# Optimization experiments

Hardware: AMD Instinct MI355X
Metric: run time of the kernel (lower is better)

The kernel has to match this reference:

```python
import jax, jax.numpy as jnp
import numpy as np
from jax import lax

B, N = 4, 5  # batches, cavs per batch (record_len fixed to 5)
SHAPES = [(64, 128, 256), (128, 64, 128), (256, 32, 64)]  # (C,H,W) per scale


def _base_grid(H, W, align_corners):
    if align_corners:
        xs = jnp.linspace(-1.0, 1.0, W)
        ys = jnp.linspace(-1.0, 1.0, H)
    else:
        xs = (jnp.arange(W, dtype=jnp.float32) + 0.5) * (2.0 / W) - 1.0
        ys = (jnp.arange(H, dtype=jnp.float32) + 0.5) * (2.0 / H) - 1.0
    gx, gy = jnp.meshgrid(xs, ys)  # [H,W] each, x varies along W
    return jnp.stack([gx, gy], axis=-1)  # [H,W,2]


def affine_grid(theta, H, W, align_corners):
    # theta: [M,2,3]  -> grid [M,H,W,2], matches torch.F.affine_grid
    base = _base_grid(H, W, align_corners)
    coords = jnp.concatenate([base, jnp.ones((H, W, 1), base.dtype)], axis=-1)  # [H,W,3]
    return jnp.einsum('nij,hwj->nhwi', theta, coords)


def grid_sample(img, grid, align_corners):
    # img [M,C,H,W], grid [M,Hg,Wg,2]; bilinear, zero padding (torch defaults)
    M, C, H, W = img.shape
    gx, gy = grid[..., 0], grid[..., 1]
    if align_corners:
        ix = (gx + 1.0) * 0.5 * (W - 1)
        iy = (gy + 1.0) * 0.5 * (H - 1)
    else:
        ix = ((gx + 1.0) * W - 1.0) * 0.5
        iy = ((gy + 1.0) * H - 1.0) * 0.5
    x0 = jnp.floor(ix); y0 = jnp.floor(iy)
    x1 = x0 + 1.0;      y1 = y0 + 1.0
    wx1 = ix - x0; wx0 = 1.0 - wx1
    wy1 = iy - y0; wy0 = 1.0 - wy1

    def sample_corner(im, xx, yy):
        valid = ((xx >= 0) & (xx < W) & (yy >= 0) & (yy < H)).astype(im.dtype)
        xc = jnp.clip(xx, 0, W - 1).astype(jnp.int32)
        yc = jnp.clip(yy, 0, H - 1).astype(jnp.int32)
        return im[:, yc, xc] * valid[None]  # [C,Hg,Wg]

    def per_image(im, x0_, x1_, y0_, y1_, w00, w01, w10, w11):
        return (sample_corner(im, x0_, y0_) * w00[None]
                + sample_corner(im, x1_, y0_) * w01[None]
                + sample_corner(im, x0_, y1_) * w10[None]
                + sample_corner(im, x1_, y1_) * w11[None])

    return jax.vmap(per_image)(img, x0, x1, y0, y1, wx0 * wy0, wx1 * wy0, wx0 * wy1, wx1 * wy1)


def conv2d(x, w, b, pad):
    y = lax.conv_general_dilated(x, w, (1, 1), [(pad, pad), (pad, pad)],
                                 dimension_numbers=('NCHW', 'OIHW', 'NCHW'))
    return y + b[None, :, None, None]


def instance_norm(x, eps=1e-5):  # torch InstanceNorm2d(affine=False)
    m = jnp.mean(x, axis=(2, 3), keepdims=True)
    v = jnp.var(x, axis=(2, 3), keepdims=True)
    return (x - m) * lax.rsqrt(v + eps)


def leaky(x):
    return jnp.where(x >= 0, x, 0.01 * x)


def setup_inputs():
    key = jax.random.key(0)
    ks = jax.random.split(key, 8)
    out = {}
    for i, (C, H, W) in enumerate(SHAPES):
        out[f'feat{i}'] = jax.random.normal(ks[i], (B * N, C, H, W), dtype=jnp.float32)
    eye = jnp.array([[1., 0., 0.], [0., 1., 0.]], dtype=jnp.float32)
    out['pairwise_t_matrix'] = (jnp.broadcast_to(eye, (B, N, N, 2, 3))
                                + 0.02 * jax.random.normal(ks[3], (B, N, N, 2, 3), dtype=jnp.float32))
    out['record_len'] = jnp.full((B,), N, dtype=jnp.int32)
    C0 = SHAPES[0][0]
    def w(k, shape, fan):
        return jax.random.normal(k, shape, jnp.float32) * (1.0 / np.sqrt(fan))
    out['w1'] = w(ks[4], (32, 2 * C0, 3, 3), 2 * C0 * 9); out['b1'] = jnp.zeros((32,), jnp.float32)
    out['w2'] = w(ks[5], (16, 32, 3, 3), 32 * 9);          out['b2'] = jnp.zeros((16,), jnp.float32)
    out['w3'] = w(ks[6], (8, 16, 1, 1), 16);               out['b3'] = jnp.zeros((8,), jnp.float32)
    out['w4'] = w(ks[7], (2, 8, 1, 1), 8) * 0.1;           out['b4'] = jnp.zeros((2,), jnp.float32)
    return out


def _forward(feat0, feat1, feat2, pairwise_t_matrix, w1, b1, w2, b2, w3, b3, w4, b4):
    feats = [feat0, feat1, feat2]
    # warp every agent into ego (i=0) frame at every scale; warp_affine_simple uses align_corners=True
    theta = pairwise_t_matrix[:, 0, :, :, :].reshape(B * N, 2, 3)
    warped = []
    for f in feats:
        C, H, W = f.shape[1:]
        g = affine_grid(theta, H, W, True)
        warped.append(grid_sample(f, g, True).reshape(B, N, C, H, W))
    C0, H0, W0 = feats[0].shape[1:]
    w0 = warped[0]
    ego = jnp.broadcast_to(w0[:, :1], (B, N - 1, C0, H0, W0))
    cat = jnp.concatenate([ego, w0[:, 1:]], axis=2).reshape(B * (N - 1), 2 * C0, H0, W0)
    # ArbitraryOffset grid net
    x = leaky(instance_norm(conv2d(cat, w1, b1, 1)))
    x = leaky(instance_norm(conv2d(x, w2, b2, 1)))
    x = leaky(instance_norm(conv2d(x, w3, b3, 0)))
    x = conv2d(x, w4, b4, 0)  # [M,2,H0,W0]
    grid_res = x.reshape(B * (N - 1), H0, W0, 2)  # faithful: raw reshape as in the torch source
    grid = grid_res + _base_grid(H0, W0, False)   # identity affine_grid (align_corners=False)
    fused = []
    for s, f in enumerate(warped):
        C, Hs, Ws = f.shape[2:]
        gs = grid[:, ::2 ** s, ::2 ** s, :]  # [M,Hs,Ws,2]
        neigh = f[:, 1:].reshape(B * (N - 1), C, Hs, Ws)
        deformed = grid_sample(neigh, gs, False).reshape(B, N - 1, C, Hs, Ws)
        fused.append(jnp.max(jnp.concatenate([deformed, f[:, :1]], axis=1), axis=1))
    return tuple(fused)


def reference(feat0, feat1, feat2, pairwise_t_matrix, record_len, w1, b1, w2, b2, w3, b3, w4, b4):
    # record_len is fixed to N per batch (constant); kept for signature fidelity
    return _forward(feat0, feat1, feat2, pairwise_t_matrix, w1, b1, w2, b2, w3, b3, w4, b4)
```

## Files before the change

### kernel.cpp

```cpp
#include <hip/hip_runtime.h>


struct Bilin { int i00, i01, i10, i11; float w00, w01, w10, w11; };

__device__ __forceinline__ Bilin make_bilin(float ix, float iy, int W, int H) {
    float x0f = floorf(ix), y0f = floorf(iy);
    float wx1 = ix - x0f, wy1 = iy - y0f;
    float wx0 = 1.f - wx1, wy0 = 1.f - wy1;
    int x0 = (int)x0f, y0 = (int)y0f;
    int x1 = x0 + 1, y1 = y0 + 1;
    bool vx0 = (x0 >= 0 && x0 < W), vx1 = (x1 >= 0 && x1 < W);
    bool vy0 = (y0 >= 0 && y0 < H), vy1 = (y1 >= 0 && y1 < H);
    int cx0 = min(max(x0, 0), W - 1), cx1 = min(max(x1, 0), W - 1);
    int cy0 = min(max(y0, 0), H - 1), cy1 = min(max(y1, 0), H - 1);
    Bilin b;
    b.i00 = cy0 * W + cx0; b.i01 = cy0 * W + cx1;
    b.i10 = cy1 * W + cx0; b.i11 = cy1 * W + cx1;
    b.w00 = (vx0 && vy0) ? wx0 * wy0 : 0.f;
    b.w01 = (vx1 && vy0) ? wx1 * wy0 : 0.f;
    b.w10 = (vx0 && vy1) ? wx0 * wy1 : 0.f;
    b.w11 = (vx1 && vy1) ? wx1 * wy1 : 0.f;
    return b;
}

__global__ __launch_bounds__(256) void warp_kernel(
    const float* __restrict__ src, const float* __restrict__ tmat,
    float* __restrict__ dst, int C, int H, int W)
{
    int idx = blockIdx.x * 256 + threadIdx.x;
    int CGn = C >> 4;
    int HW = H * W;
    int total = 20 * CGn * HW;
    if (idx >= total) return;
    int w   = idx % W;
    int h   = (idx / W) % H;
    int cg  = (idx / HW) % CGn;
    int img = idx / (HW * CGn);
    int b = img / 5, n = img % 5;
    const float* th = tmat + (b * 25 + n) * 6;
    float gx = -1.f + 2.f * w / (float)(W - 1);
    float gy = -1.f + 2.f * h / (float)(H - 1);
    float tx = th[0] * gx + th[1] * gy + th[2];
    float ty = th[3] * gx + th[4] * gy + th[5];
    float ix = (tx + 1.f) * 0.5f * (W - 1);
    float iy = (ty + 1.f) * 0.5f * (H - 1);
    Bilin bl = make_bilin(ix, iy, W, H);
    const float* im = src + ((size_t)img * C + cg * 16) * HW;
    float* op = dst + ((size_t)img * C + cg * 16) * HW + h * W + w;
    #pragma unroll 4
    for (int c = 0; c < 16; ++c) {
        const float* pl = im + c * HW;
        op[c * HW] = pl[bl.i00] * bl.w00 + pl[bl.i01] * bl.w01 +
                     pl[bl.i10] * bl.w10 + pl[bl.i11] * bl.w11;
    }
}

__global__ __launch_bounds__(256) void stats_kernel(
    const float* __restrict__ x, float* __restrict__ stats, int HW)
{
    int pc = blockIdx.x;
    const float* p = x + (size_t)pc * HW;
    float s = 0.f, s2 = 0.f;
    for (int i = threadIdx.x; i < HW; i += 256) {
        float v = p[i];
        s += v; s2 += v * v;
    }
    __shared__ float ss[256], sq[256];
    ss[threadIdx.x] = s; sq[threadIdx.x] = s2;
    __syncthreads();
    for (int o = 128; o > 0; o >>= 1) {
        if (threadIdx.x < o) {
            ss[threadIdx.x] += ss[threadIdx.x + o];
            sq[threadIdx.x] += sq[threadIdx.x + o];
        }
        __syncthreads();
    }
    if (threadIdx.x == 0) {
        float m = ss[0] / HW;
        float var = sq[0] / HW - m * m;
        stats[pc * 2]     = m;
        stats[pc * 2 + 1] = rsqrtf(var + 1e-5f);
    }
}

template<int CIN, int COUT, int WSTRIDE, int SRC, bool INIT, bool NORM>
__global__ __launch_bounds__(256) void conv3x3v2(
    const float* __restrict__ src, const float* __restrict__ wgt,
    const float* __restrict__ bias, const float* __restrict__ stats,
    const float* __restrict__ init, float* __restrict__ dst)
{
    constexpr int H = 128, W = 256, HW = H * W;
    constexpr int CHUNK = 8;
    constexpr int OCP = COUT / 4;
    constexpr int PW = 68;
    __shared__ __align__(16) float s_in[CHUNK][10][PW];
    __shared__ __align__(16) float s_w[CHUNK * 9 * COUT];

    int tid = threadIdx.x;
    int bi  = blockIdx.x;
    int p   = bi >> 6;
    int rem = bi & 63;
    int h_base = (rem >> 2) * 8;
    int w_base = (rem & 3) * 64;
    int cg = tid >> 6;
    int sg = tid & 63;
    int r  = sg >> 3;
    int cw = (sg & 7) * 8;

    float acc[OCP][8];
    #pragma unroll
    for (int o = 0; o < OCP; ++o)
        #pragma unroll
        for (int i = 0; i < 8; ++i) acc[o][i] = 0.f;

    for (int ci = 0; ci < CIN / CHUNK; ++ci) {
        if (ci) __syncthreads();
        for (int t = tid; t < CHUNK * 10 * 66; t += 256) {
            int c   = t / 660;
            int r2  = t % 660;
            int row = r2 / 66, col = r2 % 66;
            int gy = h_base + row - 1, gxx = w_base + col - 1;
            float v = 0.f;
            if (gy >= 0 && gy < H && gxx >= 0 && gxx < W) {
                int cglob = ci * CHUNK + c;
                const float* plane;
                if (SRC == 1) {
                    plane = src + ((size_t)(p * 5) * 64 + cglob) * HW;
                } else if (SRC == 2) {
                    int bb = p >> 2, jm = p & 3;
                    plane = src + ((size_t)(bb * 5 + 1 + jm) * 64 + cglob) * HW;
                } else {
                    plane = src + ((size_t)p * CIN + cglob) * HW;
                }
                v = plane[gy * W + gxx];
                if (NORM) {
                    float m  = stats[(p * CIN + cglob) * 2];
                    float rs = stats[(p * CIN + cglob) * 2 + 1];
                    v = (v - m) * rs;
                    v = v >= 0.f ? v : 0.01f * v;
                }
            }
            s_in[c][row][col] = v;
        }
        for (int t = tid; t < CHUNK * 9 * COUT; t += 256) {
            int c   = t / (9 * COUT);
            int pos = (t / COUT) % 9;
            int o   = t % COUT;
            s_w[(c * 9 + pos) * COUT + o] =
                wgt[((size_t)o * WSTRIDE + ci * CHUNK + c) * 9 + pos];
        }
        __syncthreads();
        #pragma unroll 1
        for (int c = 0; c < CHUNK; ++c) {
            float in[3][10];
            #pragma unroll
            for (int dy = 0; dy < 3; ++dy) {
                const float* rp = &s_in[c][r + dy][cw];
                float4 a = *reinterpret_cast<const float4*>(rp);
                float4 b = *reinterpret_cast<const float4*>(rp + 4);
                float2 e = *reinterpret_cast<const float2*>(rp + 8);
                in[dy][0] = a.x; in[dy][1] = a.y; in[dy][2] = a.z; in[dy][3] = a.w;
                in[dy][4] = b.x; in[dy][5] = b.y; in[dy][6] = b.z; in[dy][7] = b.w;
                in[dy][8] = e.x; in[dy][9] = e.y;
            }
            const float* wp = &s_w[c * 9 * COUT + cg * OCP];
            #pragma unroll
            for (int dy = 0; dy < 3; ++dy) {
                #pragma unroll
                for (int dx = 0; dx < 3; ++dx) {
                    float wv[OCP];
                    #pragma unroll
                    for (int o = 0; o < OCP; o += 4) {
                        float4 wq = *reinterpret_cast<const float4*>(wp + (dy * 3 + dx) * COUT + o);
                        wv[o] = wq.x; wv[o + 1] = wq.y; wv[o + 2] = wq.z; wv[o + 3] = wq.w;
                    }
                    #pragma unroll
                    for (int o = 0; o < OCP; ++o)
                        #pragma unroll
                        for (int px = 0; px < 8; ++px)
                            acc[o][px] = fmaf(in[dy][dx + px], wv[o], acc[o][px]);
                }
            }
        }
    }
    int hh = h_base + r, ww = w_base + cw;
    #pragma unroll
    for (int o = 0; o < OCP; ++o) {
        int oc = cg * OCP + o;
        float bv = (SRC == 1) ? 0.f : bias[oc];
        float add[8];
        #pragma unroll
        for (int i = 0; i < 8; ++i) add[i] = bv;
        if (INIT) {
            int bb = (SRC == 2) ? (p >> 2) : p;
            const float* ip = init + ((size_t)bb * COUT + oc) * HW + hh * W + ww;
            float4 e0 = *reinterpret_cast<const float4*>(ip);
            float4 e1 = *reinterpret_cast<const float4*>(ip + 4);
            add[0] += e0.x; add[1] += e0.y; add[2] += e0.z; add[3] += e0.w;
            add[4] += e1.x; add[5] += e1.y; add[6] += e1.z; add[7] += e1.w;
        }
        float* op = dst + (((size_t)p * COUT + oc) * H + hh) * W + ww;
        float4 v0 = make_float4(acc[o][0] + add[0], acc[o][1] + add[1],
                                acc[o][2] + add[2], acc[o][3] + add[3]);
        float4 v1 = make_float4(acc[o][4] + add[4], acc[o][5] + add[5],
                                acc[o][6] + add[6], acc[o][7] + add[7]);
        *reinterpret_cast<float4*>(op)     = v0;
        *reinterpret_cast<float4*>(op + 4) = v1;
    }
}

template<int CIN, int COUT>
__global__ __launch_bounds__(256) void conv1x1_kernel(
    const float* __restrict__ src, const float* __restrict__ wgt,
    const float* __restrict__ bias, const float* __restrict__ stats,
    float* __restrict__ dst)
{
    constexpr int HW = 128 * 256;
    __shared__ float s_w[COUT * CIN];
    __shared__ float s_b[COUT];
    int tid = threadIdx.x;
    for (int t = tid; t < COUT * CIN; t += 256) s_w[t] = wgt[t];
    if (tid < COUT) s_b[tid] = bias[tid];
    __syncthreads();
    int p  = blockIdx.x >> 7;
    int px = ((blockIdx.x & 127) << 8) + tid;
    float in[CIN];
    #pragma unroll
    for (int c = 0; c < CIN; ++c) {
        float v  = src[((size_t)p * CIN + c) * HW + px];
        float m  = stats[(p * CIN + c) * 2];
        float rs = stats[(p * CIN + c) * 2 + 1];
        v = (v - m) * rs;
        in[c] = v >= 0.f ? v : 0.01f * v;
    }
    #pragma unroll
    for (int o = 0; o < COUT; ++o) {
        float s = s_b[o];
        #pragma unroll
        for (int c = 0; c < CIN; ++c) s = fmaf(in[c], s_w[o * CIN + c], s);
        dst[((size_t)p * COUT + o) * HW + px] = s;
    }
}

__global__ __launch_bounds__(256) void fuse_kernel(
    const float* __restrict__ warped, const float* __restrict__ grid,
    float* __restrict__ out, int C, int Hs, int Ws, int shift)
{
    int idx = blockIdx.x * 256 + threadIdx.x;
    int CGn = C >> 4;
    int HW = Hs * Ws;
    int total = 4 * CGn * HW;
    if (idx >= total) return;
    int w  = idx % Ws;
    int h  = (idx / Ws) % Hs;
    int cg = (idx / HW) % CGn;
    int b  = idx / (HW * CGn);
    int h0 = h << shift, w0 = w << shift;
    float bx = (w0 + 0.5f) * (2.f / 256.f) - 1.f;
    float by = (h0 + 0.5f) * (2.f / 128.f) - 1.f;
    Bilin bl[4];
    #pragma unroll
    for (int j = 0; j < 4; ++j) {
        int p = b * 4 + j;
        const float* g = grid + (size_t)p * 65536 + (size_t)(h0 * 256 + w0) * 2;
        float fx = g[0] + bx;
        float fy = g[1] + by;
        float ix = ((fx + 1.f) * Ws - 1.f) * 0.5f;
        float iy = ((fy + 1.f) * Hs - 1.f) * 0.5f;
        bl[j] = make_bilin(ix, iy, Ws, Hs);
    }
    size_t egoOff = ((size_t)(b * 5) * C + cg * 16) * HW;
    float* op = out + ((size_t)b * C + cg * 16) * HW + h * Ws + w;
    for (int c = 0; c < 16; ++c) {
        float m = warped[egoOff + (size_t)c * HW + h * Ws + w];
        #pragma unroll
        for (int j = 0; j < 4; ++j) {
            const float* pl = warped + ((size_t)(b * 5 + 1 + j) * C + cg * 16 + c) * HW;
            float s = pl[bl[j].i00] * bl[j].w00 + pl[bl[j].i01] * bl[j].w01 +
                      pl[bl[j].i10] * bl[j].w10 + pl[bl[j].i11] * bl[j].w11;
            m = fmaxf(m, s);
        }
        op[(size_t)c * HW] = m;
    }
}

extern "C" void kernel_launch(void* const* d_in, const int* in_sizes, int n_in,
                              void* d_out, int out_size, void* d_ws, size_t ws_size,
                              hipStream_t stream)
{
    const float* feat0 = (const float*)d_in[0];
    const float* feat1 = (const float*)d_in[1];
    const float* feat2 = (const float*)d_in[2];
    const float* tmat  = (const float*)d_in[3];
    const float* w1 = (const float*)d_in[5];
    const float* b1 = (const float*)d_in[6];
    const float* w2 = (const float*)d_in[7];
    const float* b2 = (const float*)d_in[8];
    const float* w3 = (const float*)d_in[9];
    const float* b3 = (const float*)d_in[10];
    const float* w4 = (const float*)d_in[11];
    const float* b4 = (const float*)d_in[12];
    float* out = (float*)d_out;
    float* ws  = (float*)d_ws;

    const size_t nW0 = 41943040;
    const size_t nW1 = 20971520;
    const size_t nW2 = 10485760;
    const size_t nX1 = 16777216;
    const size_t nX2 = 8388608;
    const size_t nX3 = 4194304;
    const size_t nG  = 2097152;
    const size_t needed = (nW0 + nW1 + nW2 + nX1 + nX2 + nX3 + nG + 2048) * 4;
    if (ws_size < needed) return;

    float* W0 = ws;
    float* W1 = W0 + nW0;
    float* W2 = W1 + nW1;
    float* X1 = W2 + nW2;
    float* X2 = X1 + nX1;
    float* X3 = X2 + nX2;
    float* G  = X3 + nX3;
    float* S  = G  + nG;
    float* E  = X2;

    warp_kernel<<<10240, 256, 0, stream>>>(feat0, tmat, W0, 64, 128, 256);
    warp_kernel<<<5120,  256, 0, stream>>>(feat1, tmat, W1, 128, 64, 128);
    warp_kernel<<<2560,  256, 0, stream>>>(feat2, tmat, W2, 256, 32, 64);

    conv3x3v2<64, 32, 128, 1, false, false><<<256,  256, 0, stream>>>(W0, w1,            b1, nullptr, nullptr, E);
    conv3x3v2<64, 32, 128, 2, true,  false><<<1024, 256, 0, stream>>>(W0, w1 + 64 * 9,   b1, nullptr, E,       X1);
    stats_kernel<<<512, 256, 0, stream>>>(X1, S, 32768);
    conv3x3v2<32, 16, 32, 0, false, true><<<1024, 256, 0, stream>>>(X1, w2, b2, S, nullptr, X2);
    stats_kernel<<<256, 256, 0, stream>>>(X2, S + 1024, 32768);
    conv1x1_kernel<16, 8><<<2048, 256, 0, stream>>>(X2, w3, b3, S + 1024, X3);
    stats_kernel<<<128, 256, 0, stream>>>(X3, S + 1536, 32768);
    conv1x1_kernel<8, 2><<<2048, 256, 0, stream>>>(X3, w4, b4, S + 1536, G);

    fuse_kernel<<<2048, 256, 0, stream>>>(W0, G, out,            64, 128, 256, 0);
    fuse_kernel<<<1024, 256, 0, stream>>>(W1, G, out + 8388608, 128,  64, 128, 1);
    fuse_kernel<<<512,  256, 0, stream>>>(W2, G, out + 12582912, 256, 32,  64, 2);
}
```

Measured before the change: 1.504 ms.

## Fuse norm stats into convs, compose warps for scales 1-2, pre-transpose weights

Instance-norm statistics are now accumulated with wave shuffles and atomics inside the conv epilogues, replacing the separate stats kernels. Conv weights are pre-transposed once and read from global memory instead of being restaged in LDS, and input tiles are register-prefetched to overlap with compute. For scales 1 and 2 the affine warp and the grid sample are composed into one kernel that reads the raw features, which removes two warp kernels and their intermediate buffers at the cost of sixteen gathers per output. Atomic accumulation makes the statistics order-nondeterministic, and the composed bilinear-of-bilinear sampling gives the same result as the two-stage reference.

```diff
diff --git a/kernel.cpp b/kernel.cpp
--- a/kernel.cpp
+++ b/kernel.cpp
@@ -21,6 +21,16 @@
     b.w10 = (vx0 && vy1) ? wx0 * wy1 : 0.f;
     b.w11 = (vx1 && vy1) ? wx1 * wy1 : 0.f;
     return b;
+}
+
+__device__ __forceinline__ Bilin affine_bilin(const float* th, int xq, int yq, int W, int H) {
+    float gx = -1.f + 2.f * xq / (float)(W - 1);
+    float gy = -1.f + 2.f * yq / (float)(H - 1);
+    float tx = th[0] * gx + th[1] * gy + th[2];
+    float ty = th[3] * gx + th[4] * gy + th[5];
+    float ix = (tx + 1.f) * 0.5f * (W - 1);
+    float iy = (ty + 1.f) * 0.5f * (H - 1);
+    return make_bilin(ix, iy, W, H);
 }
 
 __global__ __launch_bounds__(256) void warp_kernel(
@@ -55,57 +65,74 @@
     }
 }
 
-__global__ __launch_bounds__(256) void stats_kernel(
-    const float* __restrict__ x, float* __restrict__ stats, int HW)
-{
-    int pc = blockIdx.x;
-    const float* p = x + (size_t)pc * HW;
-    float s = 0.f, s2 = 0.f;
-    for (int i = threadIdx.x; i < HW; i += 256) {
-        float v = p[i];
-        s += v; s2 += v * v;
-    }
-    __shared__ float ss[256], sq[256];
-    ss[threadIdx.x] = s; sq[threadIdx.x] = s2;
-    __syncthreads();
-    for (int o = 128; o > 0; o >>= 1) {
-        if (threadIdx.x < o) {
-            ss[threadIdx.x] += ss[threadIdx.x + o];
-            sq[threadIdx.x] += sq[threadIdx.x + o];
-        }
-        __syncthreads();
-    }
-    if (threadIdx.x == 0) {
-        float m = ss[0] / HW;
-        float var = sq[0] / HW - m * m;
-        stats[pc * 2]     = m;
-        stats[pc * 2 + 1] = rsqrtf(var + 1e-5f);
-    }
-}
-
-template<int CIN, int COUT, int WSTRIDE, int SRC, bool INIT, bool NORM>
-__global__ __launch_bounds__(256) void conv3x3v2(
-    const float* __restrict__ src, const float* __restrict__ wgt,
+__global__ void zero_stats(float* s) {
+    for (int i = threadIdx.x; i < 1792; i += 256) s[i] = 0.f;
+}
+
+__global__ void finalize_stats(float* s, int n, float inv_hw) {
+    int i = threadIdx.x;
+    if (i < n) {
+        float m = s[2 * i] * inv_hw;
+        float v = s[2 * i + 1] * inv_hw - m * m;
+        s[2 * i]     = m;
+        s[2 * i + 1] = rsqrtf(v + 1e-5f);
+    }
+}
+
+__global__ void transpose_w(const float* __restrict__ w1, const float* __restrict__ w2,
+                            float* __restrict__ wt1, float* __restrict__ wt2) {
+    int t = blockIdx.x * 256 + threadIdx.x;
+    for (int i = t; i < 128 * 9 * 32; i += 32 * 256) {
+        int o = i % 32, pos = (i / 32) % 9, cin = i / 288;
+        wt1[i] = w1[o * 1152 + cin * 9 + pos];
+    }
+    for (int i = t; i < 32 * 9 * 16; i += 32 * 256) {
+        int o = i % 16, pos = (i / 16) % 9, cin = i / 144;
+        wt2[i] = w2[o * 288 + cin * 9 + pos];
+    }
+}
+
+template<int CIN, int COUT, int SRC, bool INIT, bool NORM, bool STATS>
+__global__ __launch_bounds__(256, 2) void conv3x3v3(
+    const float* __restrict__ src, const float* __restrict__ wt,
     const float* __restrict__ bias, const float* __restrict__ stats,
-    const float* __restrict__ init, float* __restrict__ dst)
+    const float* __restrict__ init, float* __restrict__ dst,
+    float* __restrict__ statacc)
 {
     constexpr int H = 128, W = 256, HW = H * W;
-    constexpr int CHUNK = 8;
+    constexpr int CHUNK = 8, NCH = CIN / CHUNK;
     constexpr int OCP = COUT / 4;
     constexpr int PW = 68;
     __shared__ __align__(16) float s_in[CHUNK][10][PW];
-    __shared__ __align__(16) float s_w[CHUNK * 9 * COUT];
-
-    int tid = threadIdx.x;
-    int bi  = blockIdx.x;
-    int p   = bi >> 6;
-    int rem = bi & 63;
+
+    int tid = threadIdx.x, bi = blockIdx.x;
+    int p = bi >> 6, rem = bi & 63;
     int h_base = (rem >> 2) * 8;
     int w_base = (rem & 3) * 64;
-    int cg = tid >> 6;
-    int sg = tid & 63;
-    int r  = sg >> 3;
-    int cw = (sg & 7) * 8;
+    int cg = tid >> 6, sg = tid & 63;
+    int r = sg >> 3, cw = (sg & 7) * 8;
+    int cg_u = __builtin_amdgcn_readfirstlane(cg);
+
+    const float* base;
+    if (SRC == 1)      base = src + (size_t)(p * 5) * 64 * HW;
+    else if (SRC == 2) { int bb = p >> 2, jm = p & 3; base = src + (size_t)((bb * 5 + 1 + jm) * 64) * HW; }
+    else               base = src + (size_t)p * CIN * HW;
+
+    int gofs[3], lofs[3];
+    unsigned pvm = 0, ivm = 0;
+    #pragma unroll
+    for (int k = 0; k < 3; ++k) {
+        int e = tid + k * 256;
+        bool pv = (e < 660);
+        int row = e / 66, col = e % 66;
+        int gy = h_base + row - 1, gx = w_base + col - 1;
+        bool iv = pv && gy >= 0 && gy < H && gx >= 0 && gx < W;
+        gofs[k] = iv ? (gy * W + gx) : 0;
+        lofs[k] = pv ? (row * PW + col) : 0;
+        pvm |= (pv ? 1u : 0u) << k;
+        ivm |= (iv ? 1u : 0u) << k;
+    }
+    float* lds = &s_in[0][0][0];
 
     float acc[OCP][8];
     #pragma unroll
@@ -113,43 +140,49 @@
         #pragma unroll
         for (int i = 0; i < 8; ++i) acc[o][i] = 0.f;
 
-    for (int ci = 0; ci < CIN / CHUNK; ++ci) {
+    float pf[3][CHUNK];
+    #pragma unroll
+    for (int k = 0; k < 3; ++k)
+        if (pvm >> k & 1)
+            #pragma unroll
+            for (int c = 0; c < CHUNK; ++c)
+                pf[k][c] = base[(size_t)c * HW + gofs[k]];
+
+    for (int ci = 0; ci < NCH; ++ci) {
         if (ci) __syncthreads();
-        for (int t = tid; t < CHUNK * 10 * 66; t += 256) {
-            int c   = t / 660;
-            int r2  = t % 660;
-            int row = r2 / 66, col = r2 % 66;
-            int gy = h_base + row - 1, gxx = w_base + col - 1;
-            float v = 0.f;
-            if (gy >= 0 && gy < H && gxx >= 0 && gxx < W) {
-                int cglob = ci * CHUNK + c;
-                const float* plane;
-                if (SRC == 1) {
-                    plane = src + ((size_t)(p * 5) * 64 + cglob) * HW;
-                } else if (SRC == 2) {
-                    int bb = p >> 2, jm = p & 3;
-                    plane = src + ((size_t)(bb * 5 + 1 + jm) * 64 + cglob) * HW;
-                } else {
-                    plane = src + ((size_t)p * CIN + cglob) * HW;
+        float mrs[NORM ? 2 * CHUNK : 1];
+        if (NORM) {
+            const float4* sp = (const float4*)(stats + (size_t)(p * CIN + ci * CHUNK) * 2);
+            #pragma unroll
+            for (int q = 0; q < CHUNK / 2; ++q) {
+                float4 v = sp[q];
+                mrs[q * 4] = v.x; mrs[q * 4 + 1] = v.y; mrs[q * 4 + 2] = v.z; mrs[q * 4 + 3] = v.w;
+            }
+        }
+        #pragma unroll
+        for (int k = 0; k < 3; ++k) {
+            if (pvm >> k & 1) {
+                #pragma unroll
+                for (int c = 0; c < CHUNK; ++c) {
+                    float v = (ivm >> k & 1) ? pf[k][c] : 0.f;
+                    if (NORM && (ivm >> k & 1)) {
+                        v = (v - mrs[2 * c]) * mrs[2 * c + 1];
+                        v = v >= 0.f ? v : 0.01f * v;
+                    }
+                    lds[c * (10 * PW) + lofs[k]] = v;
                 }
-                v = plane[gy * W + gxx];
-                if (NORM) {
-                    float m  = stats[(p * CIN + cglob) * 2];
-                    float rs = stats[(p * CIN + cglob) * 2 + 1];
-                    v = (v - m) * rs;
-                    v = v >= 0.f ? v : 0.01f * v;
-                }
-            }
-            s_in[c][row][col] = v;
-        }
-        for (int t = tid; t < CHUNK * 9 * COUT; t += 256) {
-            int c   = t / (9 * COUT);
-            int pos = (t / COUT) % 9;
-            int o   = t % COUT;
-            s_w[(c * 9 + pos) * COUT + o] =
-                wgt[((size_t)o * WSTRIDE + ci * CHUNK + c) * 9 + pos];
+            }
         }
         __syncthreads();
+        if (ci + 1 < NCH) {
+            const float* nb = base + (size_t)(ci + 1) * CHUNK * HW;
+            #pragma unroll
+            for (int k = 0; k < 3; ++k)
+                if (pvm >> k & 1)
+                    #pragma unroll
+                    for (int c = 0; c < CHUNK; ++c)
+                        pf[k][c] = nb[(size_t)c * HW + gofs[k]];
+        }
         #pragma unroll 1
         for (int c = 0; c < CHUNK; ++c) {
             float in[3][10];
@@ -163,23 +196,21 @@
                 in[dy][4] = b.x; in[dy][5] = b.y; in[dy][6] = b.z; in[dy][7] = b.w;
                 in[dy][8] = e.x; in[dy][9] = e.y;
             }
-            const float* wp = &s_w[c * 9 * COUT + cg * OCP];
-            #pragma unroll
-            for (int dy = 0; dy < 3; ++dy) {
+            const float* wp = wt + (size_t)((ci * CHUNK + c) * 9) * COUT + cg_u * OCP;
+            #pragma unroll
+            for (int pos = 0; pos < 9; ++pos) {
+                const int dy = pos / 3, dx = pos % 3;
+                float wv[OCP];
                 #pragma unroll
-                for (int dx = 0; dx < 3; ++dx) {
-                    float wv[OCP];
+                for (int oq = 0; oq < OCP; oq += 4) {
+                    float4 wq = *reinterpret_cast<const float4*>(wp + pos * COUT + oq);
+                    wv[oq] = wq.x; wv[oq + 1] = wq.y; wv[oq + 2] = wq.z; wv[oq + 3] = wq.w;
+                }
+                #pragma unroll
+                for (int o = 0; o < OCP; ++o)
                     #pragma unroll
-                    for (int o = 0; o < OCP; o += 4) {
-                        float4 wq = *reinterpret_cast<const float4*>(wp + (dy * 3 + dx) * COUT + o);
-                        wv[o] = wq.x; wv[o + 1] = wq.y; wv[o + 2] = wq.z; wv[o + 3] = wq.w;
-                    }
-                    #pragma unroll
-                    for (int o = 0; o < OCP; ++o)
-                        #pragma unroll
-                        for (int px = 0; px < 8; ++px)
-                            acc[o][px] = fmaf(in[dy][dx + px], wv[o], acc[o][px]);
-                }
+                    for (int px = 0; px < 8; ++px)
+                        acc[o][px] = fmaf(in[dy][dx + px], wv[o], acc[o][px]);
             }
         }
     }
@@ -199,25 +230,39 @@
             add[0] += e0.x; add[1] += e0.y; add[2] += e0.z; add[3] += e0.w;
             add[4] += e1.x; add[5] += e1.y; add[6] += e1.z; add[7] += e1.w;
         }
+        float vals[8];
+        #pragma unroll
+        for (int i = 0; i < 8; ++i) vals[i] = acc[o][i] + add[i];
         float* op = dst + (((size_t)p * COUT + oc) * H + hh) * W + ww;
-        float4 v0 = make_float4(acc[o][0] + add[0], acc[o][1] + add[1],
-                                acc[o][2] + add[2], acc[o][3] + add[3]);
-        float4 v1 = make_float4(acc[o][4] + add[4], acc[o][5] + add[5],
-                                acc[o][6] + add[6], acc[o][7] + add[7]);
-        *reinterpret_cast<float4*>(op)     = v0;
-        *reinterpret_cast<float4*>(op + 4) = v1;
-    }
-}
-
-template<int CIN, int COUT>
+        *reinterpret_cast<float4*>(op)     = make_float4(vals[0], vals[1], vals[2], vals[3]);
+        *reinterpret_cast<float4*>(op + 4) = make_float4(vals[4], vals[5], vals[6], vals[7]);
+        if (STATS) {
+            float s = 0.f, s2 = 0.f;
+            #pragma unroll
+            for (int i = 0; i < 8; ++i) { s += vals[i]; s2 += vals[i] * vals[i]; }
+            #pragma unroll
+            for (int off = 32; off > 0; off >>= 1) {
+                s  += __shfl_down(s, off);
+                s2 += __shfl_down(s2, off);
+            }
+            if (sg == 0) {
+                atomicAdd(&statacc[(size_t)(p * COUT + oc) * 2],     s);
+                atomicAdd(&statacc[(size_t)(p * COUT + oc) * 2 + 1], s2);
+            }
+        }
+    }
+}
+
+template<int CIN, int COUT, bool STATS>
 __global__ __launch_bounds__(256) void conv1x1_kernel(
     const float* __restrict__ src, const float* __restrict__ wgt,
     const float* __restrict__ bias, const float* __restrict__ stats,
-    float* __restrict__ dst)
+    float* __restrict__ dst, float* __restrict__ statacc)
 {
     constexpr int HW = 128 * 256;
     __shared__ float s_w[COUT * CIN];
     __shared__ float s_b[COUT];
+    __shared__ float s_part[4][2 * COUT];
     int tid = threadIdx.x;
     for (int t = tid; t < COUT * CIN; t += 256) s_w[t] = wgt[t];
     if (tid < COUT) s_b[tid] = bias[tid];
@@ -233,55 +278,146 @@
         v = (v - m) * rs;
         in[c] = v >= 0.f ? v : 0.01f * v;
     }
+    float val[COUT];
     #pragma unroll
     for (int o = 0; o < COUT; ++o) {
         float s = s_b[o];
         #pragma unroll
         for (int c = 0; c < CIN; ++c) s = fmaf(in[c], s_w[o * CIN + c], s);
+        val[o] = s;
         dst[((size_t)p * COUT + o) * HW + px] = s;
     }
-}
-
-__global__ __launch_bounds__(256) void fuse_kernel(
-    const float* __restrict__ warped, const float* __restrict__ grid,
-    float* __restrict__ out, int C, int Hs, int Ws, int shift)
-{
+    if (STATS) {
+        int wv = tid >> 6, ln = tid & 63;
+        #pragma unroll
+        for (int o = 0; o < COUT; ++o) {
+            float s = val[o], s2 = val[o] * val[o];
+            #pragma unroll
+            for (int off = 32; off > 0; off >>= 1) {
+                s  += __shfl_down(s, off);
+                s2 += __shfl_down(s2, off);
+            }
+            if (ln == 0) { s_part[wv][o * 2] = s; s_part[wv][o * 2 + 1] = s2; }
+        }
+        __syncthreads();
+        if (tid < 2 * COUT) {
+            float t = s_part[0][tid] + s_part[1][tid] + s_part[2][tid] + s_part[3][tid];
+            atomicAdd(&statacc[(size_t)p * COUT * 2 + tid], t);
+        }
+    }
+}
+
+__global__ __launch_bounds__(256) void fuse0_kernel(
+    const float* __restrict__ W0, const float* __restrict__ grid,
+    float* __restrict__ out)
+{
+    constexpr int HW = 32768;
     int idx = blockIdx.x * 256 + threadIdx.x;
-    int CGn = C >> 4;
-    int HW = Hs * Ws;
-    int total = 4 * CGn * HW;
-    if (idx >= total) return;
-    int w  = idx % Ws;
-    int h  = (idx / Ws) % Hs;
-    int cg = (idx / HW) % CGn;
-    int b  = idx / (HW * CGn);
-    int h0 = h << shift, w0 = w << shift;
+    int px = idx & 32767;
+    int cg = (idx >> 15) & 1;
+    int b  = idx >> 16;
+    int w = px & 255, h = px >> 8;
+    float bx = (w + 0.5f) * (2.f / 256.f) - 1.f;
+    float by = (h + 0.5f) * (2.f / 128.f) - 1.f;
+    Bilin bl[4];
+    #pragma unroll
+    for (int j = 0; j < 4; ++j) {
+        const float2 g = *reinterpret_cast<const float2*>(
+            grid + ((size_t)(b * 4 + j)) * 65536 + (size_t)px * 2);
+        float ix = ((g.x + bx + 1.f) * 256.f - 1.f) * 0.5f;
+        float iy = ((g.y + by + 1.f) * 128.f - 1.f) * 0.5f;
+        bl[j] = make_bilin(ix, iy, 256, 128);
+    }
+    const float* ego = W0 + ((size_t)(b * 5) * 64 + cg * 32) * HW + px;
+    float* op = out + ((size_t)b * 64 + cg * 32) * HW + px;
+    #pragma unroll 2
+    for (int c = 0; c < 32; ++c) {
+        float mx = ego[(size_t)c * HW];
+        #pragma unroll
+        for (int j = 0; j < 4; ++j) {
+            const float* pl = W0 + ((size_t)(b * 5 + 1 + j) * 64 + cg * 32 + c) * HW;
+            float s = pl[bl[j].i00] * bl[j].w00 + pl[bl[j].i01] * bl[j].w01 +
+                      pl[bl[j].i10] * bl[j].w10 + pl[bl[j].i11] * bl[j].w11;
+            mx = fmaxf(mx, s);
+        }
+        op[(size_t)c * HW] = mx;
+    }
+}
+
+template<int C, int CPT, int SH, int HS, int WS>
+__global__ __launch_bounds__(256) void fuse_comp(
+    const float* __restrict__ feat, const float* __restrict__ tmat,
+    const float* __restrict__ grid, float* __restrict__ out)
+{
+    constexpr int HW = HS * WS;
+    constexpr int NCG = C / CPT;
+    int idx = blockIdx.x * 256 + threadIdx.x;
+    if (idx >= 4 * NCG * HW) return;
+    int px = idx % HW;
+    int cg = (idx / HW) % NCG;
+    int b  = idx / (HW * NCG);
+    int w = px % WS, h = px / WS;
+
+    float m[CPT];
+    {
+        const float* th = tmat + (size_t)(b * 25) * 6;
+        float t0 = th[0], t1 = th[1], t2 = th[2], t3 = th[3], t4 = th[4], t5 = th[5];
+        float thr[6] = {t0, t1, t2, t3, t4, t5};
+        Bilin bi = affine_bilin(thr, w, h, WS, HS);
+        const float* pb = feat + ((size_t)(b * 5) * C + cg * CPT) * HW;
+        #pragma unroll 4
+        for (int c = 0; c < CPT; ++c) {
+            const float* pl = pb + (size_t)c * HW;
+            m[c] = pl[bi.i00] * bi.w00 + pl[bi.i01] * bi.w01 +
+                   pl[bi.i10] * bi.w10 + pl[bi.i11] * bi.w11;
+        }
+    }
+    int h0 = h << SH, w0 = w << SH;
     float bx = (w0 + 0.5f) * (2.f / 256.f) - 1.f;
     float by = (h0 + 0.5f) * (2.f / 128.f) - 1.f;
-    Bilin bl[4];
-    #pragma unroll
     for (int j = 0; j < 4; ++j) {
-        int p = b * 4 + j;
-        const float* g = grid + (size_t)p * 65536 + (size_t)(h0 * 256 + w0) * 2;
-        float fx = g[0] + bx;
-        float fy = g[1] + by;
-        float ix = ((fx + 1.f) * Ws - 1.f) * 0.5f;
-        float iy = ((fy + 1.f) * Hs - 1.f) * 0.5f;
-        bl[j] = make_bilin(ix, iy, Ws, Hs);
-    }
-    size_t egoOff = ((size_t)(b * 5) * C + cg * 16) * HW;
-    float* op = out + ((size_t)b * C + cg * 16) * HW + h * Ws + w;
-    for (int c = 0; c < 16; ++c) {
-        float m = warped[egoOff + (size_t)c * HW + h * Ws + w];
-        #pragma unroll
-        for (int j = 0; j < 4; ++j) {
-            const float* pl = warped + ((size_t)(b * 5 + 1 + j) * C + cg * 16 + c) * HW;
-            float s = pl[bl[j].i00] * bl[j].w00 + pl[bl[j].i01] * bl[j].w01 +
-                      pl[bl[j].i10] * bl[j].w10 + pl[bl[j].i11] * bl[j].w11;
-            m = fmaxf(m, s);
-        }
-        op[(size_t)c * HW] = m;
-    }
+        const float2 g = *reinterpret_cast<const float2*>(
+            grid + ((size_t)(b * 4 + j)) * 65536 + (size_t)(h0 * 256 + w0) * 2);
+        float ix = ((g.x + bx + 1.f) * WS - 1.f) * 0.5f;
+        float iy = ((g.y + by + 1.f) * HS - 1.f) * 0.5f;
+        float x0f = floorf(ix), y0f = floorf(iy);
+        float wx1 = ix - x0f, wy1 = iy - y0f;
+        float wx0 = 1.f - wx1, wy0 = 1.f - wy1;
+        int x0 = (int)x0f, y0 = (int)y0f, x1 = x0 + 1, y1 = y0 + 1;
+        bool vx0 = (x0 >= 0 && x0 < WS), vx1 = (x1 >= 0 && x1 < WS);
+        bool vy0 = (y0 >= 0 && y0 < HS), vy1 = (y1 >= 0 && y1 < HS);
+        int cx0 = min(max(x0, 0), WS - 1), cx1 = min(max(x1, 0), WS - 1);
+        int cy0 = min(max(y0, 0), HS - 1), cy1 = min(max(y1, 0), HS - 1);
+        float ow[4] = { (vx0 && vy0) ? wx0 * wy0 : 0.f,
+                        (vx1 && vy0) ? wx1 * wy0 : 0.f,
+                        (vx0 && vy1) ? wx0 * wy1 : 0.f,
+                        (vx1 && vy1) ? wx1 * wy1 : 0.f };
+        int qx[4] = { cx0, cx1, cx0, cx1 };
+        int qy[4] = { cy0, cy0, cy1, cy1 };
+        const float* th = tmat + (size_t)(b * 25 + 1 + j) * 6;
+        float thr[6] = { th[0], th[1], th[2], th[3], th[4], th[5] };
+        Bilin in_[4];
+        #pragma unroll
+        for (int q = 0; q < 4; ++q) {
+            in_[q] = affine_bilin(thr, qx[q], qy[q], WS, HS);
+            in_[q].w00 *= ow[q]; in_[q].w01 *= ow[q];
+            in_[q].w10 *= ow[q]; in_[q].w11 *= ow[q];
+        }
+        const float* pb = feat + ((size_t)(b * 5 + 1 + j) * C + cg * CPT) * HW;
+        #pragma unroll 2
+        for (int c = 0; c < CPT; ++c) {
+            const float* pl = pb + (size_t)c * HW;
+            float s = 0.f;
+            #pragma unroll
+            for (int q = 0; q < 4; ++q)
+                s += pl[in_[q].i00] * in_[q].w00 + pl[in_[q].i01] * in_[q].w01 +
+                     pl[in_[q].i10] * in_[q].w10 + pl[in_[q].i11] * in_[q].w11;
+            m[c] = fmaxf(m[c], s);
+        }
+    }
+    float* op = out + ((size_t)b * C + cg * CPT) * HW + px;
+    #pragma unroll
+    for (int c = 0; c < CPT; ++c) op[(size_t)c * HW] = m[c];
 }
 
 extern "C" void kernel_launch(void* const* d_in, const int* in_sizes, int n_in,
@@ -304,39 +440,40 @@
     float* ws  = (float*)d_ws;
 
     const size_t nW0 = 41943040;
-    const size_t nW1 = 20971520;
-    const size_t nW2 = 10485760;
     const size_t nX1 = 16777216;
     const size_t nX2 = 8388608;
     const size_t nX3 = 4194304;
     const size_t nG  = 2097152;
-    const size_t needed = (nW0 + nW1 + nW2 + nX1 + nX2 + nX3 + nG + 2048) * 4;
+    const size_t nS  = 2048;
+    const size_t nWT = 36864 + 4608;
+    const size_t needed = (nW0 + nX1 + nX2 + nX3 + nG + nS + nWT) * 4;
     if (ws_size < needed) return;
 
-    float* W0 = ws;
-    float* W1 = W0 + nW0;
-    float* W2 = W1 + nW1;
-    float* X1 = W2 + nW2;
-    float* X2 = X1 + nX1;
-    float* X3 = X2 + nX2;
-    float* G  = X3 + nX3;
-    float* S  = G  + nG;
-    float* E  = X2;
+    float* W0  = ws;
+    float* X1  = W0 + nW0;
+    float* X2  = X1 + nX1;
+    float* X3  = X2 + nX2;
+    float* G   = X3 + nX3;
+    float* S   = G  + nG;
+    float* WT1 = S  + nS;
+    float* WT2 = WT1 + 36864;
+    float* E   = X2;
+
+    zero_stats<<<1, 256, 0, stream>>>(S);
+    transpose_w<<<32, 256, 0, stream>>>(w1, w2, WT1, WT2);
 
     warp_kernel<<<10240, 256, 0, stream>>>(feat0, tmat, W0, 64, 128, 256);
-    warp_kernel<<<5120,  256, 0, stream>>>(feat1, tmat, W1, 128, 64, 128);
-    warp_kernel<<<2560,  256, 0, stream>>>(feat2, tmat, W2, 256, 32, 64);
-
-    conv3x3v2<64, 32, 128, 1, false, false><<<256,  256, 0, stream>>>(W0, w1,            b1, nullptr, nullptr, E);
-    conv3x3v2<64, 32, 128, 2, true,  false><<<1024, 256, 0, stream>>>(W0, w1 + 64 * 9,   b1, nullptr, E,       X1);
-    stats_kernel<<<512, 256, 0, stream>>>(X1, S, 32768);
-    conv3x3v2<32, 16, 32, 0, false, true><<<1024, 256, 0, stream>>>(X1, w2, b2, S, nullptr, X2);
-    stats_kernel<<<256, 256, 0, stream>>>(X2, S + 1024, 32768);
-    conv1x1_kernel<16, 8><<<2048, 256, 0, stream>>>(X2, w3, b3, S + 1024, X3);
-    stats_kernel<<<128, 256, 0, stream>>>(X3, S + 1536, 32768);
-    conv1x1_kernel<8, 2><<<2048, 256, 0, stream>>>(X3, w4, b4, S + 1536, G);
-
-    fuse_kernel<<<2048, 256, 0, stream>>>(W0, G, out,            64, 128, 256, 0);
-    fuse_kernel<<<1024, 256, 0, stream>>>(W1, G, out + 8388608, 128,  64, 128, 1);
-    fuse_kernel<<<512,  256, 0, stream>>>(W2, G, out + 12582912, 256, 32,  64, 2);
-}
+
+    conv3x3v3<64, 32, 1, false, false, false><<<256,  256, 0, stream>>>(W0, WT1, b1, nullptr, nullptr, E, nullptr);
+    conv3x3v3<64, 32, 2, true,  false, true ><<<1024, 256, 0, stream>>>(W0, WT1 + 8 * 8 * 9 * 32, b1, nullptr, E, X1, S);
+    finalize_stats<<<1, 512, 0, stream>>>(S, 512, 1.f / 32768.f);
+    conv3x3v3<32, 16, 0, false, true,  true ><<<1024, 256, 0, stream>>>(X1, WT2, b2, S, nullptr, X2, S + 1024);
+    finalize_stats<<<1, 256, 0, stream>>>(S + 1024, 256, 1.f / 32768.f);
+    conv1x1_kernel<16, 8, true ><<<2048, 256, 0, stream>>>(X2, w3, b3, S + 1024, X3, S + 1536);
+    finalize_stats<<<1, 128, 0, stream>>>(S + 1536, 128, 1.f / 32768.f);
+    conv1x1_kernel<8, 2, false><<<2048, 256, 0, stream>>>(X3, w4, b4, S + 1536, G, nullptr);
+
+    fuse0_kernel<<<1024, 256, 0, stream>>>(W0, G, out);
+    fuse_comp<128, 32, 1, 64, 128><<<512, 256, 0, stream>>>(feat1, tmat, G, out + 8388608);
+    fuse_comp<256, 16, 2, 32,  64><<<512, 256, 0, stream>>>(feat2, tmat, G, out + 12582912);
+}
```

Result: faster. 1.400 ms (-6.9%).
